# Optimization experiments

Measured on AMD Instinct MI355X. Metric: run time of the kernel, lower is better.

## Reference

```python
import jax, jax.numpy as jnp
import numpy as np

B, T, DIN, H = 32, 4096, 256, 256


def _log_g(x):
    # log of g(x) = where(x>=0, x+0.5, sigmoid(x)), computed stably in log space
    return jnp.where(x >= 0.0, jnp.log(jax.nn.relu(x) + 0.5), -jax.nn.softplus(-x))


def setup_inputs() -> dict:
    key = jax.random.key(0)
    ks = jax.random.split(key, 4)
    scale = (6.0 / (DIN + H)) ** 0.5  # xavier_uniform
    return {
        "x": jax.random.normal(ks[0], (B, T, DIN), dtype=jnp.float32),
        "h0": jax.random.normal(ks[1], (B, 1, H), dtype=jnp.float32),
        "Wz": jax.random.uniform(ks[2], (H, DIN), jnp.float32, -scale, scale),
        "bz": jnp.zeros((H,), jnp.float32),
        "Wh": jax.random.uniform(ks[3], (H, DIN), jnp.float32, -scale, scale),
        "bh": jnp.zeros((H,), jnp.float32),
    }


def reference(x, h0, Wz, bz, Wh, bh):
    # minGRU training path: log-space parallel scan (Heinsen scan)
    k = jnp.einsum("bti,hi->bth", x, Wz) + bz            # pre-activation of z gate
    log_z = -jax.nn.softplus(-k)                           # log sigmoid(k)
    log_coeffs = -jax.nn.softplus(k)                       # log(1 - sigmoid(k))
    log_h0 = _log_g(h0)                                    # (B,1,H)
    log_tilde_h = _log_g(jnp.einsum("bti,hi->bth", x, Wh) + bh)
    log_values = jnp.concatenate([log_h0, log_z + log_tilde_h], axis=1)  # (B,T+1,H)
    # a_star[t] = sum_{s<=t} log_coeffs[s], with a leading zero
    a_star = jnp.cumsum(jnp.pad(log_coeffs, ((0, 0), (1, 0), (0, 0))), axis=1)
    # logcumsumexp along time via associative scan with logaddexp
    lcse = jax.lax.associative_scan(jnp.logaddexp, log_values - a_star, axis=1)
    log_h = a_star + lcse                                  # (B,T+1,H)
    return jnp.exp(log_h[:, 1:])                           # (B,T,H)
```

## Files before the change

### kernel.cpp

```cpp
#include <hip/hip_runtime.h>
#include <hip/hip_fp16.h>

typedef __attribute__((ext_vector_type(8))) short short8;
typedef __attribute__((ext_vector_type(4))) float f32x4;
typedef unsigned short ushort_t;
typedef unsigned int uint_t;

#define B_SZ 32
#define T_SZ 4096
#define D_IN 256
#define H_SZ 256
#define M_SZ (B_SZ * T_SZ)
#define CHUNK 64
#define NCHUNK (T_SZ / CHUNK)

__device__ __forceinline__ ushort_t f2bf(float f) {
  unsigned int u = __float_as_uint(f);
  unsigned int r = (u + 0x7FFFu + ((u >> 16) & 1u)) >> 16;
  return (ushort_t)r;
}

__device__ __forceinline__ float sigmoidf_(float xv) {
  float e = __expf(-fabsf(xv));
  float s = 1.0f / (1.0f + e);
  return xv >= 0.0f ? s : 1.0f - s;
}

__device__ __forceinline__ float unpack_lo(uint_t pk) {
  return __half2float(__ushort_as_half((ushort_t)(pk & 0xFFFFu)));
}
__device__ __forceinline__ float unpack_hi(uint_t pk) {
  return __half2float(__ushort_as_half((ushort_t)(pk >> 16)));
}

__global__ void prep_w(const float* __restrict__ Wz, const float* __restrict__ Wh,
                       ushort_t* __restrict__ wsB) {
  int g = blockIdx.x * 256 + threadIdx.x;
  if (g >= 8 * 2048) return;
  int ks = g >> 11;
  int r = g & 2047;
  int c = r >> 9;
  int n = r & 511;
  int h = (n >> 5) * 16 + (n & 15);
  const float* W = ((n >> 4) & 1) ? Wh : Wz;
  const float* src = W + (size_t)h * D_IN + ks * 32 + c * 8;
  ushort_t* dst = wsB + (size_t)g * 8;
#pragma unroll
  for (int j = 0; j < 8; ++j) dst[j] = f2bf(src[j]);
}

__global__ __launch_bounds__(512, 4) void gemm_av(
    const float* __restrict__ x, const ushort_t* __restrict__ wsB,
    const float* __restrict__ bz, const float* __restrict__ bh,
    uint_t* __restrict__ av) {
  __shared__ __align__(16) unsigned char lds[73728];
  ushort_t* As = (ushort_t*)lds;
  ushort_t* Bs = (ushort_t*)(lds + 8192);

  const int tid = threadIdx.x;
  const int lane = tid & 63;
  const int wid = tid >> 6;
  const int m0 = blockIdx.x * 64;

  const int a_row = tid & 63;
  const int a_g = tid >> 6;
  const float* asrc = x + (size_t)(m0 + a_row) * D_IN + a_g * 8;

  f32x4 acc[4][4];
#pragma unroll
  for (int rt = 0; rt < 4; ++rt)
#pragma unroll
    for (int ct = 0; ct < 4; ++ct) {
      f32x4 z4 = {0.f, 0.f, 0.f, 0.f};
      acc[rt][ct] = z4;
    }

  {
    const ushort_t* bsrc = wsB + (size_t)wid * 2048 + lane * 8;
    ushort_t* bdst = Bs + wid * 2048;
#pragma unroll
    for (int cc = 0; cc < 4; ++cc) {
      __builtin_amdgcn_global_load_lds(
          (const __attribute__((address_space(1))) void*)(bsrc + cc * 512),
          (__attribute__((address_space(3))) void*)(bdst + cc * 512), 16, 0, 0);
    }
    if (tid < 256) {
      float4 f0 = *(const float4*)(asrc);
      float4 f1 = *(const float4*)(asrc + 4);
      union { ushort_t e[8]; short8 s; } cv;
      cv.e[0] = f2bf(f0.x); cv.e[1] = f2bf(f0.y);
      cv.e[2] = f2bf(f0.z); cv.e[3] = f2bf(f0.w);
      cv.e[4] = f2bf(f1.x); cv.e[5] = f2bf(f1.y);
      cv.e[6] = f2bf(f1.z); cv.e[7] = f2bf(f1.w);
      *(short8*)(As + tid * 8) = cv.s;
    }
  }
  __syncthreads();

#pragma unroll
  for (int ks = 0; ks < 8; ++ks) {
    const int cur = ks & 1;
    short8 afr[4], bfr[4];
    {
      const int c = lane >> 4;
      const int r16 = lane & 15;
#pragma unroll
      for (int rt = 0; rt < 4; ++rt) {
        int row = rt * 16 + r16;
        afr[rt] = *(const short8*)(As + cur * 2048 + (c * 64 + row) * 8);
      }
#pragma unroll
      for (int ct = 0; ct < 4; ++ct) {
        int n = wid * 64 + ct * 16 + r16;
        bfr[ct] = *(const short8*)(Bs + cur * 16384 + (c * 512 + n) * 8);
      }
    }
    float4 nf0, nf1;
    if (ks < 7) {
      const ushort_t* bsrc = wsB + (size_t)(ks + 1) * 16384 + wid * 2048 + lane * 8;
      ushort_t* bdst = Bs + (cur ^ 1) * 16384 + wid * 2048;
#pragma unroll
      for (int cc = 0; cc < 4; ++cc) {
        __builtin_amdgcn_global_load_lds(
            (const __attribute__((address_space(1))) void*)(bsrc + cc * 512),
            (__attribute__((address_space(3))) void*)(bdst + cc * 512), 16, 0, 0);
      }
      if (tid < 256) {
        nf0 = *(const float4*)(asrc + (ks + 1) * 32);
        nf1 = *(const float4*)(asrc + (ks + 1) * 32 + 4);
      }
    }
#pragma unroll
    for (int rt = 0; rt < 4; ++rt)
#pragma unroll
      for (int ct = 0; ct < 4; ++ct)
        acc[rt][ct] = __builtin_amdgcn_mfma_f32_16x16x32_bf16(
            afr[rt], bfr[ct], acc[rt][ct], 0, 0, 0);
    if (ks < 7 && tid < 256) {
      union { ushort_t e[8]; short8 s; } cv;
      cv.e[0] = f2bf(nf0.x); cv.e[1] = f2bf(nf0.y);
      cv.e[2] = f2bf(nf0.z); cv.e[3] = f2bf(nf0.w);
      cv.e[4] = f2bf(nf1.x); cv.e[5] = f2bf(nf1.y);
      cv.e[6] = f2bf(nf1.z); cv.e[7] = f2bf(nf1.w);
      *(short8*)(As + (cur ^ 1) * 2048 + tid * 8) = cv.s;
    }
    __syncthreads();
  }

  const int col16 = lane & 15;
  const int rgrp = lane >> 4;
#pragma unroll
  for (int i = 0; i < 2; ++i) {
    int hh = (wid * 2 + i) * 16 + col16;
    float bzv = bz[hh];
    float bhv = bh[hh];
#pragma unroll
    for (int rt = 0; rt < 4; ++rt) {
#pragma unroll
      for (int j = 0; j < 4; ++j) {
        int row = m0 + rt * 16 + rgrp * 4 + j;
        float kv = acc[rt][2 * i][j] + bzv;
        float pv = acc[rt][2 * i + 1][j] + bhv;
        float a = __builtin_amdgcn_rcpf(1.0f + __expf(kv));
        float z = 1.0f - a;
        float gsig = 1.0f - __builtin_amdgcn_rcpf(1.0f + __expf(pv));
        float gg = fmaxf(pv + 0.5f, gsig);
        float vv = z * gg;
        uint_t pk = (uint_t)__half_as_ushort(__float2half_rn(a)) |
                    ((uint_t)__half_as_ushort(__float2half_rn(vv)) << 16);
        av[(size_t)row * H_SZ + hh] = pk;
      }
    }
  }
}

__global__ __launch_bounds__(256) void chunk_reduce(
    const uint_t* __restrict__ av, float2* __restrict__ cAV) {
  const int b = blockIdx.x >> 6;
  const int c = blockIdx.x & 63;
  const int h = threadIdx.x;
  const uint_t* p = av + ((size_t)b * T_SZ + c * CHUNK) * H_SZ + h;

  uint_t buf[CHUNK];
#pragma unroll
  for (int s = 0; s < CHUNK; ++s) buf[s] = p[(size_t)s * H_SZ];

  float A = 1.0f, V = 0.0f;
#pragma unroll
  for (int s = 0; s < CHUNK; ++s) {
    float a = unpack_lo(buf[s]);
    float v = unpack_hi(buf[s]);
    A = a * A;
    V = fmaf(a, V, v);
  }
  float2 r; r.x = A; r.y = V;
  cAV[((size_t)b * NCHUNK + c) * H_SZ + h] = r;
}

__global__ __launch_bounds__(256) void chunk_carry(
    const float* __restrict__ h0, const float2* __restrict__ cAV,
    float* __restrict__ hb) {
  const int b = blockIdx.x;
  const int h = threadIdx.x;
  float v0 = h0[b * H_SZ + h];
  float hc = (v0 >= 0.0f) ? (v0 + 0.5f) : sigmoidf_(v0);

  const float2* p = cAV + (size_t)b * NCHUNK * H_SZ + h;
  float* o = hb + (size_t)b * NCHUNK * H_SZ + h;

  float2 buf[NCHUNK];
#pragma unroll
  for (int c = 0; c < NCHUNK; ++c) buf[c] = p[(size_t)c * H_SZ];

#pragma unroll
  for (int c = 0; c < NCHUNK; ++c) {
    o[(size_t)c * H_SZ] = hc;
    hc = fmaf(buf[c].x, hc, buf[c].y);
  }
}

__global__ __launch_bounds__(256) void chunk_scan_out(
    const uint_t* av, const float* __restrict__ hb, float* out) {
  const int b = blockIdx.x >> 6;
  const int c = blockIdx.x & 63;
  const int h = threadIdx.x;

  float hc = hb[((size_t)b * NCHUNK + c) * H_SZ + h];
  const uint_t* p = av + ((size_t)b * T_SZ + c * CHUNK) * H_SZ + h;
  float* o = out + ((size_t)b * T_SZ + c * CHUNK) * H_SZ + h;

  uint_t buf[CHUNK];
#pragma unroll
  for (int s = 0; s < CHUNK; ++s) buf[s] = p[(size_t)s * H_SZ];

#pragma unroll
  for (int s = 0; s < CHUNK; ++s) {
    float a = unpack_lo(buf[s]);
    float v = unpack_hi(buf[s]);
    hc = fmaf(a, hc, v);
    o[(size_t)s * H_SZ] = hc;
  }
}

__global__ __launch_bounds__(64) void scan_seq(const float* __restrict__ h0,
                                               const uint_t* av, float* out) {
  const int b = blockIdx.x >> 2;
  const int hg = blockIdx.x & 3;
  const int h = hg * 64 + threadIdx.x;

  float v0 = h0[b * H_SZ + h];
  float hc = (v0 >= 0.0f) ? (v0 + 0.5f) : sigmoidf_(v0);

  const uint_t* p = av + (size_t)b * T_SZ * H_SZ + h;
  float* o = out + (size_t)b * T_SZ * H_SZ + h;

  uint_t buf[32];
#pragma unroll
  for (int d = 0; d < 32; ++d) buf[d] = p[(size_t)d * H_SZ];

  for (int t0 = 0; t0 < T_SZ; t0 += 32) {
#pragma unroll
    for (int d = 0; d < 32; ++d) {
      int t = t0 + d;
      uint_t pk = buf[d];
      int tn = t + 32;
      if (tn < T_SZ) buf[d] = p[(size_t)tn * H_SZ];
      hc = fmaf(unpack_lo(pk), hc, unpack_hi(pk));
      o[(size_t)t * H_SZ] = hc;
    }
  }
}

extern "C" void kernel_launch(void* const* d_in, const int* in_sizes, int n_in,
                              void* d_out, int out_size, void* d_ws, size_t ws_size,
                              hipStream_t stream) {
  const float* x  = (const float*)d_in[0];
  const float* h0 = (const float*)d_in[1];
  const float* Wz = (const float*)d_in[2];
  const float* bz = (const float*)d_in[3];
  const float* Wh = (const float*)d_in[4];
  const float* bh = (const float*)d_in[5];
  float* out = (float*)d_out;

  const size_t wsBBytes = 262144;
  const size_t cavBytes = (size_t)B_SZ * NCHUNK * H_SZ * 8;
  const size_t hbBytes  = (size_t)B_SZ * NCHUNK * H_SZ * 4;
  const size_t avOff    = 8388608;
  const size_t avBytes  = (size_t)M_SZ * H_SZ * 4;

  ushort_t* wsB = (ushort_t*)d_ws;
  float2* cAV = (float2*)((char*)d_ws + wsBBytes);
  float* hb   = (float*)((char*)d_ws + wsBBytes + cavBytes);

  const bool haveSummaries = ws_size >= wsBBytes + cavBytes + hbBytes;
  uint_t* av;
  if (ws_size >= avOff + avBytes) {
    av = (uint_t*)((char*)d_ws + avOff);
  } else {
    av = (uint_t*)d_out;
  }

  prep_w<<<64, 256, 0, stream>>>(Wz, Wh, wsB);
  gemm_av<<<M_SZ / 64, 512, 0, stream>>>(x, wsB, bz, bh, av);
  if (haveSummaries) {
    chunk_reduce<<<B_SZ * NCHUNK, 256, 0, stream>>>(av, cAV);
    chunk_carry<<<B_SZ, 256, 0, stream>>>(h0, cAV, hb);
    chunk_scan_out<<<B_SZ * NCHUNK, 256, 0, stream>>>(av, hb, out);
  } else {
    scan_seq<<<B_SZ * 4, 64, 0, stream>>>(h0, av, out);
  }
}
```

Before: 196.2 us.

## Fuse per-chunk scan summary into GEMM epilogue, drop chunk_reduce kernel

The GEMM epilogue now computes each 64-row chunk's (A,V) scan summary in registers with cross-lane shuffles and writes it straight to cAV. This removes the separate chunk_reduce kernel and its full re-read of the av buffer. The gate math also switches to the branchy sigmoid helper. The costs are extra shuffles and ALU work in the epilogue, and the summaries are built from fp32 values rather than the fp16-rounded ones that the later scan reads, which could shift numerics slightly.

```diff
diff --git a/kernel.cpp b/kernel.cpp
--- a/kernel.cpp
+++ b/kernel.cpp
@@ -52,7 +52,7 @@
 __global__ __launch_bounds__(512, 4) void gemm_av(
     const float* __restrict__ x, const ushort_t* __restrict__ wsB,
     const float* __restrict__ bz, const float* __restrict__ bh,
-    uint_t* __restrict__ av) {
+    uint_t* __restrict__ av, float2* cAV) {
   __shared__ __align__(16) unsigned char lds[73728];
   ushort_t* As = (ushort_t*)lds;
   ushort_t* Bs = (ushort_t*)(lds + 8192);
@@ -154,47 +154,41 @@
     int hh = (wid * 2 + i) * 16 + col16;
     float bzv = bz[hh];
     float bhv = bh[hh];
+    float CA = 1.0f, CV = 0.0f;
 #pragma unroll
     for (int rt = 0; rt < 4; ++rt) {
+      float A4 = 1.0f, V4 = 0.0f;
 #pragma unroll
       for (int j = 0; j < 4; ++j) {
         int row = m0 + rt * 16 + rgrp * 4 + j;
         float kv = acc[rt][2 * i][j] + bzv;
         float pv = acc[rt][2 * i + 1][j] + bhv;
-        float a = __builtin_amdgcn_rcpf(1.0f + __expf(kv));
+        float a = sigmoidf_(-kv);
         float z = 1.0f - a;
-        float gsig = 1.0f - __builtin_amdgcn_rcpf(1.0f + __expf(pv));
-        float gg = fmaxf(pv + 0.5f, gsig);
+        float gg = (pv >= 0.0f) ? (pv + 0.5f) : sigmoidf_(pv);
         float vv = z * gg;
         uint_t pk = (uint_t)__half_as_ushort(__float2half_rn(a)) |
                     ((uint_t)__half_as_ushort(__float2half_rn(vv)) << 16);
         av[(size_t)row * H_SZ + hh] = pk;
-      }
-    }
-  }
-}
-
-__global__ __launch_bounds__(256) void chunk_reduce(
-    const uint_t* __restrict__ av, float2* __restrict__ cAV) {
-  const int b = blockIdx.x >> 6;
-  const int c = blockIdx.x & 63;
-  const int h = threadIdx.x;
-  const uint_t* p = av + ((size_t)b * T_SZ + c * CHUNK) * H_SZ + h;
-
-  uint_t buf[CHUNK];
-#pragma unroll
-  for (int s = 0; s < CHUNK; ++s) buf[s] = p[(size_t)s * H_SZ];
-
-  float A = 1.0f, V = 0.0f;
-#pragma unroll
-  for (int s = 0; s < CHUNK; ++s) {
-    float a = unpack_lo(buf[s]);
-    float v = unpack_hi(buf[s]);
-    A = a * A;
-    V = fmaf(a, V, v);
-  }
-  float2 r; r.x = A; r.y = V;
-  cAV[((size_t)b * NCHUNK + c) * H_SZ + h] = r;
+        V4 = fmaf(a, V4, vv);
+        A4 *= a;
+      }
+      float Ap = __shfl_xor(A4, 16);
+      float Vp = __shfl_xor(V4, 16);
+      float A8 = A4 * Ap;
+      float V8 = (lane & 16) ? fmaf(A4, Vp, V4) : fmaf(Ap, V4, Vp);
+      float Ap2 = __shfl_xor(A8, 32);
+      float Vp2 = __shfl_xor(V8, 32);
+      float A16 = A8 * Ap2;
+      float V16 = (lane & 32) ? fmaf(A8, Vp2, V8) : fmaf(Ap2, V8, Vp2);
+      CV = fmaf(A16, CV, V16);
+      CA = CA * A16;
+    }
+    if (cAV != nullptr && lane < 16) {
+      float2 r; r.x = CA; r.y = CV;
+      cAV[(size_t)blockIdx.x * H_SZ + hh] = r;
+    }
+  }
 }
 
 __global__ __launch_bounds__(256) void chunk_carry(
@@ -301,9 +295,9 @@
   }
 
   prep_w<<<64, 256, 0, stream>>>(Wz, Wh, wsB);
-  gemm_av<<<M_SZ / 64, 512, 0, stream>>>(x, wsB, bz, bh, av);
+  gemm_av<<<M_SZ / 64, 512, 0, stream>>>(x, wsB, bz, bh, av,
+                                         haveSummaries ? cAV : (float2*)nullptr);
   if (haveSummaries) {
-    chunk_reduce<<<B_SZ * NCHUNK, 256, 0, stream>>>(av, cAV);
     chunk_carry<<<B_SZ, 256, 0, stream>>>(h0, cAV, hb);
     chunk_scan_out<<<B_SZ * NCHUNK, 256, 0, stream>>>(av, hb, out);
   } else {
```

Result: faster. 163.4 us (-16.7%).
